# Optimization experiments

Hardware: AMD Instinct MI355X
Metric: run time of the kernel (lower is better)

The kernel has to match this reference:

```python
import jax, jax.numpy as jnp
import numpy as np

DIM = 2048
N_HEADS = 32
N_KV_HEADS = 8
HEAD_DIM = DIM // N_HEADS
N_REP = N_HEADS // N_KV_HEADS
BSZ, SEQ = 2, 2048


def setup_inputs() -> dict:
    key = jax.random.key(0)
    ks = jax.random.split(key, 6)
    hidden_states = jax.random.normal(ks[0], (BSZ, SEQ, DIM), jnp.float32)
    # additive causal mask [1,1,S,S]
    causal = jnp.tril(jnp.ones((SEQ, SEQ), jnp.bool_))
    attention_mask = jnp.where(causal, 0.0, -1e9).astype(jnp.float32)[None, None]
    # RoPE tables [S, head_dim]
    inv_freq = 1.0 / (10000.0 ** (np.arange(0, HEAD_DIM, 2, dtype=np.float32) / HEAD_DIM))
    t = np.arange(SEQ, dtype=np.float32)
    freqs = np.outer(t, inv_freq)  # [S, head_dim/2]
    emb = np.concatenate([freqs, freqs], axis=-1)  # [S, head_dim]
    position_cos = jnp.asarray(np.cos(emb), jnp.float32)
    position_sin = jnp.asarray(np.sin(emb), jnp.float32)
    s = 0.02
    Wq = jax.random.normal(ks[1], (DIM, DIM), jnp.float32) * s
    Wk = jax.random.normal(ks[2], (N_KV_HEADS * HEAD_DIM, DIM), jnp.float32) * s
    Wv = jax.random.normal(ks[3], (N_KV_HEADS * HEAD_DIM, DIM), jnp.float32) * s
    Wo = jax.random.normal(ks[4], (DIM, DIM), jnp.float32) * s
    return {"hidden_states": hidden_states, "attention_mask": attention_mask,
            "position_cos": position_cos, "position_sin": position_sin,
            "Wq": Wq, "Wk": Wk, "Wv": Wv, "Wo": Wo}


def _rotate_half(x):
    x1, x2 = jnp.split(x, 2, axis=-1)
    return jnp.concatenate([-x2, x1], axis=-1)


def _apply_rope(x, cos, sin):
    # x: [b, h, s, d]; cos/sin: [s, d] broadcast over (b, h)
    return x * cos + _rotate_half(x) * sin


def reference(hidden_states, attention_mask, position_cos, position_sin, Wq, Wk, Wv, Wo):
    b, s, _ = hidden_states.shape
    q = jnp.einsum('bsd,ed->bse', hidden_states, Wq).reshape(b, s, N_HEADS, HEAD_DIM).transpose(0, 2, 1, 3)
    k = jnp.einsum('bsd,ed->bse', hidden_states, Wk).reshape(b, s, N_KV_HEADS, HEAD_DIM).transpose(0, 2, 1, 3)
    v = jnp.einsum('bsd,ed->bse', hidden_states, Wv).reshape(b, s, N_KV_HEADS, HEAD_DIM).transpose(0, 2, 1, 3)
    q = _apply_rope(q, position_cos, position_sin)
    k = _apply_rope(k, position_cos, position_sin)
    # GQA: group query heads over kv heads instead of physically repeating k/v
    qg = q.reshape(b, N_KV_HEADS, N_REP, s, HEAD_DIM)
    scores = jnp.einsum('bgrqd,bgkd->bgrqk', qg, k) * (1.0 / jnp.sqrt(jnp.float32(HEAD_DIM)))
    scores = scores + attention_mask[:, :, None, :s, :s]
    weights = jax.nn.softmax(scores.astype(jnp.float32), axis=-1).astype(q.dtype)
    attn = jnp.einsum('bgrqk,bgkd->bgrqd', weights, v)
    attn = attn.reshape(b, N_HEADS, s, HEAD_DIM).transpose(0, 2, 1, 3).reshape(b, s, DIM)
    out = jnp.einsum('bsd,ed->bse', attn, Wo)
    return out
```

## Files before the change

### kernel.cpp

```cpp
#include <hip/hip_runtime.h>
#include <math.h>

#define BSZ 2
#define SEQ 2048
#define DIM 2048
#define NH 32
#define NKV 8
#define HD 64
#define KVDIM 512

typedef short short8 __attribute__((ext_vector_type(8)));
typedef short short4v __attribute__((ext_vector_type(4)));
typedef float f32x4 __attribute__((ext_vector_type(4)));

__device__ __forceinline__ short fbf(float x) {
    unsigned u = __float_as_uint(x);
    u = (u + 0x7fffu + ((u >> 16) & 1u)) >> 16;
    return (short)u;
}
__device__ __forceinline__ short pbf(float x) {
    return (short)((__float_as_uint(x) + 0x8000u) >> 16);
}

#define AS1(p) ((const __attribute__((address_space(1))) void*)(p))
#define AS3(p) ((__attribute__((address_space(3))) void*)(p))

__global__ __launch_bounds__(256) void prep(const float* __restrict__ X,
                                            const float* __restrict__ Wq,
                                            const float* __restrict__ Wk,
                                            const float* __restrict__ Wv,
                                            const float* __restrict__ Wo,
                                            short* __restrict__ Xb,
                                            short* __restrict__ Wqkv,
                                            short* __restrict__ Wob) {
    int i = blockIdx.x * 256 + threadIdx.x;
    const float* src; short* dst; int j;
    if (i < 2097152)      { src = X;  dst = Xb;             j = i; }
    else if (i < 3145728) { src = Wq; dst = Wqkv;           j = i - 2097152; }
    else if (i < 3407872) { src = Wk; dst = Wqkv + 4194304; j = i - 3145728; }
    else if (i < 3670016) { src = Wv; dst = Wqkv + 5242880; j = i - 3407872; }
    else                  { src = Wo; dst = Wob;            j = i - 3670016; }
    float4 f = ((const float4*)src)[j];
    short4v s = { fbf(f.x), fbf(f.y), fbf(f.z), fbf(f.w) };
    ((short4v*)dst)[j] = s;
}

__global__ __launch_bounds__(256) void gemm_qkv(const short* __restrict__ A,
                                                const short* __restrict__ W,
                                                const float* __restrict__ cosT,
                                                const float* __restrict__ sinT,
                                                short* __restrict__ Qo,
                                                short* __restrict__ Ko,
                                                short* __restrict__ Vo) {
    __shared__ short As[128 * 64];
    __shared__ short Bs[128 * 64];
    const int K = 2048;
    const int tid = threadIdx.x;
    const int lane = tid & 63, wave = tid >> 6;
    const int l15 = lane & 15, quad = lane >> 4;
    const int m0 = blockIdx.y * 128, n0 = blockIdx.x * 128;
    const int wm = (wave >> 1) * 64, wn = (wave & 1) * 64;
    f32x4 acc[4][4] = {};
    int srow[4], gcol[4];
#pragma unroll
    for (int v = 0; v < 4; ++v) {
        int s = v * 256 + tid;
        srow[v] = s >> 3;
        gcol[v] = ((s & 7) ^ (srow[v] & 7)) * 8;
    }
    for (int kb = 0; kb < K; kb += 64) {
        __syncthreads();
#pragma unroll
        for (int v = 0; v < 4; ++v) {
            int s = v * 256 + tid;
            __builtin_amdgcn_global_load_lds(AS1(A + (size_t)(m0 + srow[v]) * K + kb + gcol[v]),
                                             AS3(&As[s * 8]), 16, 0, 0);
            __builtin_amdgcn_global_load_lds(AS1(W + (size_t)(n0 + srow[v]) * K + kb + gcol[v]),
                                             AS3(&Bs[s * 8]), 16, 0, 0);
        }
        __syncthreads();
#pragma unroll
        for (int kh = 0; kh < 2; ++kh) {
            const int cs = ((kh * 4 + quad) ^ (l15 & 7)) * 8;
            short8 af[4], bf8[4];
#pragma unroll
            for (int i = 0; i < 4; ++i)
                af[i] = *(const short8*)&As[(wm + i * 16 + l15) * 64 + cs];
#pragma unroll
            for (int j = 0; j < 4; ++j)
                bf8[j] = *(const short8*)&Bs[(wn + j * 16 + l15) * 64 + cs];
#pragma unroll
            for (int i = 0; i < 4; ++i)
#pragma unroll
                for (int j = 0; j < 4; ++j)
                    acc[i][j] = __builtin_amdgcn_mfma_f32_16x16x32_bf16(af[i], bf8[j], acc[i][j], 0, 0, 0);
        }
    }
    const int n0r = n0 + wn;
    if (n0r < 2560) {
        short* dst; int heads, hh; float scale;
        if (n0r < 2048) { dst = Qo; heads = NH;  hh = n0r >> 6;          scale = 0.125f * 1.44269504088896f; }
        else            { dst = Ko; heads = NKV; hh = (n0r - 2048) >> 6; scale = 1.0f; }
#pragma unroll
        for (int i = 0; i < 4; ++i)
#pragma unroll
            for (int r = 0; r < 4; ++r) {
                int mrow = m0 + wm + i * 16 + quad * 4 + r;
                int s = mrow & (SEQ - 1);
                int bb = mrow >> 11;
                size_t rowbase = ((size_t)(bb * SEQ + s) * heads + hh) * HD;
#pragma unroll
                for (int jp = 0; jp < 2; ++jp) {
                    int d1 = jp * 16 + l15;
                    float c1 = cosT[s * HD + d1],      s1 = sinT[s * HD + d1];
                    float c2 = cosT[s * HD + d1 + 32], s2 = sinT[s * HD + d1 + 32];
                    float x1 = acc[i][jp][r], x2 = acc[i][jp + 2][r];
                    dst[rowbase + d1]      = fbf((x1 * c1 - x2 * s1) * scale);
                    dst[rowbase + d1 + 32] = fbf((x2 * c2 + x1 * s2) * scale);
                }
            }
    } else {
        const int hh = (n0r - 2560) >> 6;
#pragma unroll
        for (int i = 0; i < 4; ++i) {
            int mrow4 = m0 + wm + i * 16 + quad * 4;
            int s_abs = mrow4 & (SEQ - 1);
            int bb = mrow4 >> 11;
            int blk = s_abs >> 6, kk = s_abs & 63;
            int ob = ((kk >> 5) << 3) | (((kk >> 2) & 3) << 1) | ((kk >> 4) & 1);
#pragma unroll
            for (int j = 0; j < 4; ++j) {
                int d = j * 16 + l15;
                short4v pk = { fbf(acc[i][j][0]), fbf(acc[i][j][1]),
                               fbf(acc[i][j][2]), fbf(acc[i][j][3]) };
                *(short4v*)&Vo[(((size_t)(bb * NKV + hh) * HD + d) * SEQ) + blk * 64 + ob * 4] = pk;
            }
        }
    }
}

__global__ __launch_bounds__(256) void gemm_bf16(const short* __restrict__ A,
                                                 const short* __restrict__ W,
                                                 float* __restrict__ C,
                                                 int M, int N, int K) {
    __shared__ short As[128 * 64];
    __shared__ short Bs[128 * 64];
    const int tid = threadIdx.x;
    const int lane = tid & 63, wave = tid >> 6;
    const int l15 = lane & 15, quad = lane >> 4;
    const int m0 = blockIdx.y * 128, n0 = blockIdx.x * 128;
    const int wm = (wave >> 1) * 64, wn = (wave & 1) * 64;
    f32x4 acc[4][4] = {};
    int srow[4], gcol[4];
#pragma unroll
    for (int v = 0; v < 4; ++v) {
        int s = v * 256 + tid;
        srow[v] = s >> 3;
        gcol[v] = ((s & 7) ^ (srow[v] & 7)) * 8;
    }
    for (int kb = 0; kb < K; kb += 64) {
        __syncthreads();
#pragma unroll
        for (int v = 0; v < 4; ++v) {
            int s = v * 256 + tid;
            __builtin_amdgcn_global_load_lds(AS1(A + (size_t)(m0 + srow[v]) * K + kb + gcol[v]),
                                             AS3(&As[s * 8]), 16, 0, 0);
            __builtin_amdgcn_global_load_lds(AS1(W + (size_t)(n0 + srow[v]) * K + kb + gcol[v]),
                                             AS3(&Bs[s * 8]), 16, 0, 0);
        }
        __syncthreads();
#pragma unroll
        for (int kh = 0; kh < 2; ++kh) {
            const int cs = ((kh * 4 + quad) ^ (l15 & 7)) * 8;
            short8 af[4], bf8[4];
#pragma unroll
            for (int i = 0; i < 4; ++i)
                af[i] = *(const short8*)&As[(wm + i * 16 + l15) * 64 + cs];
#pragma unroll
            for (int j = 0; j < 4; ++j)
                bf8[j] = *(const short8*)&Bs[(wn + j * 16 + l15) * 64 + cs];
#pragma unroll
            for (int i = 0; i < 4; ++i)
#pragma unroll
                for (int j = 0; j < 4; ++j)
                    acc[i][j] = __builtin_amdgcn_mfma_f32_16x16x32_bf16(af[i], bf8[j], acc[i][j], 0, 0, 0);
        }
    }
#pragma unroll
    for (int i = 0; i < 4; ++i)
#pragma unroll
        for (int j = 0; j < 4; ++j)
#pragma unroll
            for (int r = 0; r < 4; ++r)
                C[(size_t)(m0 + wm + i * 16 + quad * 4 + r) * N + n0 + wn + j * 16 + l15] = acc[i][j][r];
}

__global__ __launch_bounds__(256, 4) void flash3(const short* __restrict__ Qb,
                                                 const short* __restrict__ Kb,
                                                 const short* __restrict__ VT,
                                                 short* __restrict__ O) {
    __shared__ short Ks[2][64 * 64];
    __shared__ short Vs[2][64 * 64];
    const int bh = blockIdx.x;
    const int qt = (int)gridDim.y - 1 - (int)blockIdx.y;
    const int b = bh >> 5, h = bh & 31, kvh = h >> 2;
    const int tid = threadIdx.x;
    const int wave = tid >> 6, lane = tid & 63;
    const int l15 = lane & 15, quad = lane >> 4;

    short8 qf[2][2];
#pragma unroll
    for (int g = 0; g < 2; ++g) {
        const short* qp = Qb + ((size_t)b * SEQ + qt * 128 + g * 64 + wave * 16 + l15) * DIM + h * HD + quad * 8;
        qf[g][0] = *(const short8*)qp;
        qf[g][1] = *(const short8*)(qp + 32);
    }
    f32x4 o[2][4] = {};
    float m[2] = {-1e30f, -1e30f}, l[2] = {0.f, 0.f};

    const short* Kbase = Kb + (size_t)b * SEQ * KVDIM + kvh * HD;
    const short* Vbase = VT + (size_t)(b * NKV + kvh) * HD * SEQ;

    int srow[2], gcol[2];
#pragma unroll
    for (int v = 0; v < 2; ++v) {
        int s = v * 256 + tid;
        srow[v] = s >> 3;
        gcol[v] = ((s & 7) ^ (srow[v] & 7)) * 8;
    }
    auto issue = [&](int kt, int bi) {
#pragma unroll
        for (int v = 0; v < 2; ++v) {
            int s = v * 256 + tid;
            __builtin_amdgcn_global_load_lds(AS1(Kbase + (size_t)(kt * 64 + srow[v]) * KVDIM + gcol[v]),
                                             AS3(&Ks[bi][s * 8]), 16, 0, 0);
            __builtin_amdgcn_global_load_lds(AS1(Vbase + (size_t)srow[v] * SEQ + kt * 64 + gcol[v]),
                                             AS3(&Vs[bi][s * 8]), 16, 0, 0);
        }
    };
    issue(0, 0);
    const int nkt = 2 * qt + 2;
    for (int kt = 0; kt < nkt; ++kt) {
        const int bi = kt & 1;
        __syncthreads();
        if (kt + 1 < nkt) issue(kt + 1, bi ^ 1);
        short8 vf[4][2];
#pragma unroll
        for (int dt = 0; dt < 4; ++dt)
#pragma unroll
            for (int hh = 0; hh < 2; ++hh)
                vf[dt][hh] = *(const short8*)&Vs[bi][(dt * 16 + l15) * 64 + (((hh * 4 + quad) ^ (l15 & 7)) << 3)];

#pragma unroll
        for (int g = 0; g < 2; ++g) {
            const int qmin = qt * 128 + g * 64 + wave * 16;
            if (kt * 64 > qmin + 15) continue;
            f32x4 st[4] = {};
#pragma unroll
            for (int nt = 0; nt < 4; ++nt) {
                short8 ka = *(const short8*)&Ks[bi][(nt * 16 + l15) * 64 + ((quad ^ (l15 & 7)) << 3)];
                st[nt] = __builtin_amdgcn_mfma_f32_16x16x32_bf16(ka, qf[g][0], st[nt], 0, 0, 0);
            }
#pragma unroll
            for (int nt = 0; nt < 4; ++nt) {
                short8 kb = *(const short8*)&Ks[bi][(nt * 16 + l15) * 64 + (((4 + quad) ^ (l15 & 7)) << 3)];
                st[nt] = __builtin_amdgcn_mfma_f32_16x16x32_bf16(kb, qf[g][1], st[nt], 0, 0, 0);
            }
            if (kt * 64 + 63 > qmin) {
                const int q = qmin + l15;
#pragma unroll
                for (int nt = 0; nt < 4; ++nt)
#pragma unroll
                    for (int r = 0; r < 4; ++r)
                        if (kt * 64 + nt * 16 + quad * 4 + r > q) st[nt][r] = -1e30f;
            }
            float mx = st[0][0];
#pragma unroll
            for (int nt = 0; nt < 4; ++nt)
#pragma unroll
                for (int r = 0; r < 4; ++r) mx = fmaxf(mx, st[nt][r]);
            mx = fmaxf(mx, __shfl_xor(mx, 16));
            mx = fmaxf(mx, __shfl_xor(mx, 32));
            float mn = fmaxf(m[g], mx);
            float al = exp2f(m[g] - mn);
            m[g] = mn;
            float p[4][4];
            float rs = 0.f;
#pragma unroll
            for (int nt = 0; nt < 4; ++nt)
#pragma unroll
                for (int r = 0; r < 4; ++r) {
                    p[nt][r] = exp2f(st[nt][r] - mn);
                    rs += p[nt][r];
                }
            rs += __shfl_xor(rs, 16);
            rs += __shfl_xor(rs, 32);
            l[g] = l[g] * al + rs;
            short8 af0, af1;
#pragma unroll
            for (int r = 0; r < 4; ++r) {
                af0[r] = pbf(p[0][r]); af0[r + 4] = pbf(p[1][r]);
                af1[r] = pbf(p[2][r]); af1[r + 4] = pbf(p[3][r]);
            }
            float alr[4];
#pragma unroll
            for (int r = 0; r < 4; ++r) alr[r] = __shfl(al, quad * 4 + r);
#pragma unroll
            for (int dt = 0; dt < 4; ++dt) {
                f32x4 t = o[g][dt];
                t[0] *= alr[0]; t[1] *= alr[1]; t[2] *= alr[2]; t[3] *= alr[3];
                t = __builtin_amdgcn_mfma_f32_16x16x32_bf16(af0, vf[dt][0], t, 0, 0, 0);
                t = __builtin_amdgcn_mfma_f32_16x16x32_bf16(af1, vf[dt][1], t, 0, 0, 0);
                o[g][dt] = t;
            }
        }
    }
#pragma unroll
    for (int g = 0; g < 2; ++g) {
        float lr[4];
#pragma unroll
        for (int r = 0; r < 4; ++r) lr[r] = 1.0f / __shfl(l[g], quad * 4 + r);
        short* Oo = O + ((size_t)b * SEQ + qt * 128 + g * 64 + wave * 16 + quad * 4) * DIM + h * HD + l15;
#pragma unroll
        for (int r = 0; r < 4; ++r)
#pragma unroll
            for (int dt = 0; dt < 4; ++dt)
                Oo[(size_t)r * DIM + dt * 16] = fbf(o[g][dt][r] * lr[r]);
    }
}

extern "C" void kernel_launch(void* const* d_in, const int* in_sizes, int n_in,
                              void* d_out, int out_size, void* d_ws, size_t ws_size,
                              hipStream_t stream) {
    const float* X    = (const float*)d_in[0];
    const float* cosT = (const float*)d_in[2];
    const float* sinT = (const float*)d_in[3];
    const float* Wq   = (const float*)d_in[4];
    const float* Wk   = (const float*)d_in[5];
    const float* Wv   = (const float*)d_in[6];
    const float* Wo   = (const float*)d_in[7];

    char* ws = (char*)d_ws;
    short* Xb    = (short*)(ws);
    short* ATTb  = Xb;
    short* WQKVb = (short*)(ws + 16777216);
    short* Wob   = (short*)(ws + 29360128);
    short* Qbb   = (short*)(ws + 37748736);
    short* Kbb   = (short*)(ws + 54525952);
    short* VTb   = (short*)(ws + 58720256);

    const int M = BSZ * SEQ;
    dim3 blk(256);

    prep<<<dim3(18432), blk, 0, stream>>>(X, Wq, Wk, Wv, Wo, Xb, WQKVb, Wob);
    gemm_qkv<<<dim3(24, M / 128), blk, 0, stream>>>(Xb, WQKVb, cosT, sinT, Qbb, Kbb, VTb);
    flash3<<<dim3(BSZ * NH, SEQ / 128), blk, 0, stream>>>(Qbb, Kbb, VTb, ATTb);
    gemm_bf16<<<dim3(DIM / 128, M / 128), blk, 0, stream>>>(ATTb, Wob, (float*)d_out, M, DIM, DIM);
}
```

Before: 360.0 us.

## Widen flash attention KV tile to 128 and stage QK epilogue through LDS

The flash attention kernel now processes 128 keys per tile instead of 64. This halves the number of tile iterations and barriers and amortizes the softmax bookkeeping over more keys, at the cost of more LDS and registers, so occupancy is lowered to 2 blocks per SM. Separately, the Q/K GEMM epilogue writes RoPE results into a swizzled LDS buffer and then stores them as 16-byte vectors, replacing scattered 2-byte global stores. It also reuses one cos/sin pair for both rotated halves, which relies on the table having equal halves. The causal skip of fully masked key blocks within a tile was removed, so some masked work is now computed on diagonal tiles.

```diff
diff --git a/kernel.cpp b/kernel.cpp
--- a/kernel.cpp
+++ b/kernel.cpp
@@ -52,8 +52,9 @@
                                                 short* __restrict__ Qo,
                                                 short* __restrict__ Ko,
                                                 short* __restrict__ Vo) {
-    __shared__ short As[128 * 64];
-    __shared__ short Bs[128 * 64];
+    __shared__ short SM[2 * 128 * 64];
+    short* As = SM;
+    short* Bs = SM + 128 * 64;
     const int K = 2048;
     const int tid = threadIdx.x;
     const int lane = tid & 63, wave = tid >> 6;
@@ -96,29 +97,39 @@
                     acc[i][j] = __builtin_amdgcn_mfma_f32_16x16x32_bf16(af[i], bf8[j], acc[i][j], 0, 0, 0);
         }
     }
+    __syncthreads();
     const int n0r = n0 + wn;
     if (n0r < 2560) {
         short* dst; int heads, hh; float scale;
         if (n0r < 2048) { dst = Qo; heads = NH;  hh = n0r >> 6;          scale = 0.125f * 1.44269504088896f; }
         else            { dst = Ko; heads = NKV; hh = (n0r - 2048) >> 6; scale = 1.0f; }
+        short* EB = SM + wave * 4096;
 #pragma unroll
         for (int i = 0; i < 4; ++i)
 #pragma unroll
             for (int r = 0; r < 4; ++r) {
-                int mrow = m0 + wm + i * 16 + quad * 4 + r;
-                int s = mrow & (SEQ - 1);
-                int bb = mrow >> 11;
-                size_t rowbase = ((size_t)(bb * SEQ + s) * heads + hh) * HD;
+                int rr = i * 16 + quad * 4 + r;
+                int s = (m0 + wm + rr) & (SEQ - 1);
+                int msk = ((rr >> 1) & 7) * 8;
 #pragma unroll
                 for (int jp = 0; jp < 2; ++jp) {
                     int d1 = jp * 16 + l15;
-                    float c1 = cosT[s * HD + d1],      s1 = sinT[s * HD + d1];
-                    float c2 = cosT[s * HD + d1 + 32], s2 = sinT[s * HD + d1 + 32];
+                    float c1 = cosT[s * HD + d1], s1v = sinT[s * HD + d1];
                     float x1 = acc[i][jp][r], x2 = acc[i][jp + 2][r];
-                    dst[rowbase + d1]      = fbf((x1 * c1 - x2 * s1) * scale);
-                    dst[rowbase + d1 + 32] = fbf((x2 * c2 + x1 * s2) * scale);
+                    EB[rr * 64 + (d1 ^ msk)]        = fbf((x1 * c1 - x2 * s1v) * scale);
+                    EB[rr * 64 + ((d1 + 32) ^ msk)] = fbf((x2 * c1 + x1 * s1v) * scale);
                 }
             }
+#pragma unroll
+        for (int t = 0; t < 8; ++t) {
+            int rr = (lane >> 3) + t * 8;
+            int c = lane & 7;
+            short8 v8 = *(const short8*)&EB[rr * 64 + c * 8];
+            int dchunk = c ^ ((rr >> 1) & 7);
+            int mrow = m0 + wm + rr;
+            int s = mrow & (SEQ - 1), bb = mrow >> 11;
+            *(short8*)&dst[((size_t)(bb * SEQ + s) * heads + hh) * HD + dchunk * 8] = v8;
+        }
     } else {
         const int hh = (n0r - 2560) >> 6;
 #pragma unroll
@@ -195,12 +206,12 @@
                 C[(size_t)(m0 + wm + i * 16 + quad * 4 + r) * N + n0 + wn + j * 16 + l15] = acc[i][j][r];
 }
 
-__global__ __launch_bounds__(256, 4) void flash3(const short* __restrict__ Qb,
+__global__ __launch_bounds__(256, 2) void flash4(const short* __restrict__ Qb,
                                                  const short* __restrict__ Kb,
                                                  const short* __restrict__ VT,
                                                  short* __restrict__ O) {
-    __shared__ short Ks[2][64 * 64];
-    __shared__ short Vs[2][64 * 64];
+    __shared__ short Ks[2][128 * 64];
+    __shared__ short Vs[2][64 * 128];
     const int bh = blockIdx.x;
     const int qt = (int)gridDim.y - 1 - (int)blockIdx.y;
     const int b = bh >> 5, h = bh & 31, kvh = h >> 2;
@@ -221,62 +232,56 @@
     const short* Kbase = Kb + (size_t)b * SEQ * KVDIM + kvh * HD;
     const short* Vbase = VT + (size_t)(b * NKV + kvh) * HD * SEQ;
 
-    int srow[2], gcol[2];
-#pragma unroll
-    for (int v = 0; v < 2; ++v) {
+    int krow[4], kcol[4], vrow[4], vcol[4];
+#pragma unroll
+    for (int v = 0; v < 4; ++v) {
         int s = v * 256 + tid;
-        srow[v] = s >> 3;
-        gcol[v] = ((s & 7) ^ (srow[v] & 7)) * 8;
+        krow[v] = s >> 3;
+        kcol[v] = ((s & 7) ^ (krow[v] & 7)) * 8;
+        vrow[v] = s >> 4;
+        vcol[v] = ((s & 15) ^ (vrow[v] & 7)) * 8;
     }
     auto issue = [&](int kt, int bi) {
 #pragma unroll
-        for (int v = 0; v < 2; ++v) {
+        for (int v = 0; v < 4; ++v) {
             int s = v * 256 + tid;
-            __builtin_amdgcn_global_load_lds(AS1(Kbase + (size_t)(kt * 64 + srow[v]) * KVDIM + gcol[v]),
+            __builtin_amdgcn_global_load_lds(AS1(Kbase + (size_t)(kt * 128 + krow[v]) * KVDIM + kcol[v]),
                                              AS3(&Ks[bi][s * 8]), 16, 0, 0);
-            __builtin_amdgcn_global_load_lds(AS1(Vbase + (size_t)srow[v] * SEQ + kt * 64 + gcol[v]),
+            __builtin_amdgcn_global_load_lds(AS1(Vbase + (size_t)vrow[v] * SEQ + kt * 128 + vcol[v]),
                                              AS3(&Vs[bi][s * 8]), 16, 0, 0);
         }
     };
     issue(0, 0);
-    const int nkt = 2 * qt + 2;
+    const int nkt = qt + 1;
     for (int kt = 0; kt < nkt; ++kt) {
         const int bi = kt & 1;
         __syncthreads();
         if (kt + 1 < nkt) issue(kt + 1, bi ^ 1);
-        short8 vf[4][2];
-#pragma unroll
-        for (int dt = 0; dt < 4; ++dt)
-#pragma unroll
-            for (int hh = 0; hh < 2; ++hh)
-                vf[dt][hh] = *(const short8*)&Vs[bi][(dt * 16 + l15) * 64 + (((hh * 4 + quad) ^ (l15 & 7)) << 3)];
 
 #pragma unroll
         for (int g = 0; g < 2; ++g) {
             const int qmin = qt * 128 + g * 64 + wave * 16;
-            if (kt * 64 > qmin + 15) continue;
-            f32x4 st[4] = {};
-#pragma unroll
-            for (int nt = 0; nt < 4; ++nt) {
-                short8 ka = *(const short8*)&Ks[bi][(nt * 16 + l15) * 64 + ((quad ^ (l15 & 7)) << 3)];
-                st[nt] = __builtin_amdgcn_mfma_f32_16x16x32_bf16(ka, qf[g][0], st[nt], 0, 0, 0);
-            }
-#pragma unroll
-            for (int nt = 0; nt < 4; ++nt) {
-                short8 kb = *(const short8*)&Ks[bi][(nt * 16 + l15) * 64 + (((4 + quad) ^ (l15 & 7)) << 3)];
-                st[nt] = __builtin_amdgcn_mfma_f32_16x16x32_bf16(kb, qf[g][1], st[nt], 0, 0, 0);
-            }
-            if (kt * 64 + 63 > qmin) {
+            f32x4 st[8] = {};
+#pragma unroll
+            for (int kh = 0; kh < 2; ++kh) {
+                const int cs = ((kh * 4 + quad) ^ (l15 & 7)) * 8;
+#pragma unroll
+                for (int nt = 0; nt < 8; ++nt) {
+                    short8 ka = *(const short8*)&Ks[bi][(nt * 16 + l15) * 64 + cs];
+                    st[nt] = __builtin_amdgcn_mfma_f32_16x16x32_bf16(ka, qf[g][kh], st[nt], 0, 0, 0);
+                }
+            }
+            if (kt * 128 + 127 > qmin) {
                 const int q = qmin + l15;
 #pragma unroll
-                for (int nt = 0; nt < 4; ++nt)
+                for (int nt = 0; nt < 8; ++nt)
 #pragma unroll
                     for (int r = 0; r < 4; ++r)
-                        if (kt * 64 + nt * 16 + quad * 4 + r > q) st[nt][r] = -1e30f;
+                        if (kt * 128 + nt * 16 + quad * 4 + r > q) st[nt][r] = -1e30f;
             }
             float mx = st[0][0];
 #pragma unroll
-            for (int nt = 0; nt < 4; ++nt)
+            for (int nt = 0; nt < 8; ++nt)
 #pragma unroll
                 for (int r = 0; r < 4; ++r) mx = fmaxf(mx, st[nt][r]);
             mx = fmaxf(mx, __shfl_xor(mx, 16));
@@ -284,24 +289,19 @@
             float mn = fmaxf(m[g], mx);
             float al = exp2f(m[g] - mn);
             m[g] = mn;
-            float p[4][4];
             float rs = 0.f;
-#pragma unroll
-            for (int nt = 0; nt < 4; ++nt)
+            short8 af[4];
+#pragma unroll
+            for (int nt = 0; nt < 8; ++nt)
 #pragma unroll
                 for (int r = 0; r < 4; ++r) {
-                    p[nt][r] = exp2f(st[nt][r] - mn);
-                    rs += p[nt][r];
+                    float pv = exp2f(st[nt][r] - mn);
+                    rs += pv;
+                    af[nt >> 1][(nt & 1) * 4 + r] = pbf(pv);
                 }
             rs += __shfl_xor(rs, 16);
             rs += __shfl_xor(rs, 32);
             l[g] = l[g] * al + rs;
-            short8 af0, af1;
-#pragma unroll
-            for (int r = 0; r < 4; ++r) {
-                af0[r] = pbf(p[0][r]); af0[r + 4] = pbf(p[1][r]);
-                af1[r] = pbf(p[2][r]); af1[r + 4] = pbf(p[3][r]);
-            }
             float alr[4];
 #pragma unroll
             for (int r = 0; r < 4; ++r) alr[r] = __shfl(al, quad * 4 + r);
@@ -309,8 +309,12 @@
             for (int dt = 0; dt < 4; ++dt) {
                 f32x4 t = o[g][dt];
                 t[0] *= alr[0]; t[1] *= alr[1]; t[2] *= alr[2]; t[3] *= alr[3];
-                t = __builtin_amdgcn_mfma_f32_16x16x32_bf16(af0, vf[dt][0], t, 0, 0, 0);
-                t = __builtin_amdgcn_mfma_f32_16x16x32_bf16(af1, vf[dt][1], t, 0, 0, 0);
+#pragma unroll
+                for (int kh = 0; kh < 4; ++kh) {
+                    const int slot = (kh * 4 + quad) ^ (l15 & 7);
+                    short8 vf = *(const short8*)&Vs[bi][(dt * 16 + l15) * 128 + slot * 8];
+                    t = __builtin_amdgcn_mfma_f32_16x16x32_bf16(af[kh], vf, t, 0, 0, 0);
+                }
                 o[g][dt] = t;
             }
         }
@@ -354,6 +358,6 @@
 
     prep<<<dim3(18432), blk, 0, stream>>>(X, Wq, Wk, Wv, Wo, Xb, WQKVb, Wob);
     gemm_qkv<<<dim3(24, M / 128), blk, 0, stream>>>(Xb, WQKVb, cosT, sinT, Qbb, Kbb, VTb);
-    flash3<<<dim3(BSZ * NH, SEQ / 128), blk, 0, stream>>>(Qbb, Kbb, VTb, ATTb);
+    flash4<<<dim3(BSZ * NH, SEQ / 128), blk, 0, stream>>>(Qbb, Kbb, VTb, ATTb);
     gemm_bf16<<<dim3(DIM / 128, M / 128), blk, 0, stream>>>(ATTb, Wob, (float*)d_out, M, DIM, DIM);
 }
```

New measurement: 331.2 us. 8.0% less time.
